# Performance work log

Hardware: AMD Instinct MI355X
Metric: run time of the kernel (lower is better)

## Reference

```python
import jax, jax.numpy as jnp
import numpy as np

NFEATS = 768; NHIDS = 768; H = 8; HD = NHIDS // H
NT = 32768; NC = 32768; NS = 32768; DEG = 8; E = NT * DEG
ALPHA = 0.2  # LeakyReLU negative slope


def setup_inputs() -> dict:
    key = jax.random.key(0)
    ks = jax.random.split(key, 16)
    f32 = jnp.float32
    dst = jnp.repeat(jnp.arange(NT, dtype=jnp.int32), DEG)  # uniform in-degree mailbox
    return {
        'h': jax.random.normal(ks[0], (NT, NFEATS), f32),
        'hb_c_src': jax.random.normal(ks[1], (NC, NHIDS), f32),
        'hb_s_src': jax.random.normal(ks[2], (NS, NHIDS), f32),
        'Wg': jax.random.normal(ks[3], (H, NFEATS, HD), f32) * 0.05,
        'bg': jnp.zeros((H, HD), f32),
        'ag': jax.random.normal(ks[4], (H, 2 * HD), f32) * 0.1,
        'agb': jnp.zeros((H,), f32),
        'Wx': jax.random.normal(ks[5], (H, NHIDS, HD), f32) * 0.05,
        'bx': jnp.zeros((H, HD), f32),
        'ax': jax.random.normal(ks[6], (H, 2 * HD), f32) * 0.1,
        'axb': jnp.zeros((H,), f32),
        'Wih': jax.random.normal(ks[7], (3 * NHIDS, NHIDS), f32) * 0.02,
        'Whh': jax.random.normal(ks[8], (3 * NHIDS, NHIDS), f32) * 0.02,
        'bih': jnp.zeros((3 * NHIDS,), f32),
        'bhh': jnp.zeros((3 * NHIDS,), f32),
        'intra_src': jax.random.randint(ks[9], (E,), 0, NT, jnp.int32),
        'intra_dst': dst,
        'c_src': jax.random.randint(ks[10], (E,), 0, NC, jnp.int32),
        'c_dst': dst,
        's_src': jax.random.randint(ks[11], (E,), 0, NS, jnp.int32),
        's_dst': dst,
    }


def _attend(Wh_s, Wh_d, src, dst, a, ab, n_dst):
    """Multi-head GAT edge attention + segment softmax + weighted aggregation.
    Wh_s: [Ns,H,D] src projections, Wh_d: [Nd,H,D] dst projections.
    a([Wh_src||Wh_dst]) decomposed as a_src.Wh_src + a_dst.Wh_dst + bias."""
    D = Wh_s.shape[-1]
    e = (jnp.einsum('nhd,hd->nh', Wh_s, a[:, :D])[src]
         + jnp.einsum('nhd,hd->nh', Wh_d, a[:, D:])[dst] + ab)  # [E,H]
    e = jax.nn.leaky_relu(e, ALPHA)
    m = jax.ops.segment_max(e, dst, num_segments=n_dst)
    ex = jnp.exp(e - m[dst])
    den = jax.ops.segment_sum(ex, dst, num_segments=n_dst)
    att = ex / den[dst]  # per-dst softmax over incoming edges (DGL mailbox softmax)
    out = jax.ops.segment_sum(Wh_s[src] * att[..., None], dst, num_segments=n_dst)
    return out.reshape(n_dst, H * D)  # concat heads


def _forward(h, hb_c_src, hb_s_src, Wg, bg, ag, agb, Wx, bx, ax, axb,
             Wih, Whh, bih, bhh, intra_src, intra_dst, c_src, c_dst, s_src, s_dst):
    n = h.shape[0]
    # intra-turn GAT (x = self.gat(g, t)); dropout is identity in eval mode
    Wh = jnp.einsum('nf,hfd->nhd', h, Wg) + bg
    x = _attend(Wh, Wh, intra_src, intra_dst, ag, agb, n)
    # cross-turn inversed GAT; dst nodes' 'hb' feature is the fresh gat output x;
    # counter_bw and support_bw share the same xgat weights.
    Wx_d = jnp.einsum('nf,hfd->nhd', x, Wx) + bx
    Wc_s = jnp.einsum('nf,hfd->nhd', hb_c_src, Wx) + bx
    h_c = _attend(Wc_s, Wx_d, c_src, c_dst, ax, axb, n)
    Ws_s = jnp.einsum('nf,hfd->nhd', hb_s_src, Wx) + bx
    h_s = _attend(Ws_s, Wx_d, s_src, s_dst, ax, axb, n)
    hid = 0.5 * h_c + 0.5 * h_s
    # GRUCell(x, hid)
    gi = x @ Wih.T + bih
    gh = hid @ Whh.T + bhh
    ir, iz, inn = jnp.split(gi, 3, axis=1)
    hr, hz, hn = jnp.split(gh, 3, axis=1)
    r = jax.nn.sigmoid(ir + hr)
    z = jax.nn.sigmoid(iz + hz)
    cand = jnp.tanh(inn + r * hn)
    return (1.0 - z) * cand + z * hid


def reference(h, hb_c_src, hb_s_src, Wg, bg, ag, agb, Wx, bx, ax, axb,
              Wih, Whh, bih, bhh, intra_src, intra_dst, c_src, c_dst, s_src, s_dst):
    return _forward(h, hb_c_src, hb_s_src, Wg, bg, ag, agb, Wx, bx, ax, axb,
                    Wih, Whh, bih, bhh, intra_src, intra_dst, c_src, c_dst, s_src, s_dst)
```

## Files before the change

kernel.cpp:

```cpp
#include <hip/hip_runtime.h>
#include <hip/hip_bf16.h>
#include <math.h>

#define NT 32768
#define HD 96
#define DEG 8
#define NE (NT * DEG)
#define LRELU_ALPHA 0.2f
#define CH 16384

typedef __attribute__((ext_vector_type(8))) short bf16x8;
typedef __attribute__((ext_vector_type(8))) unsigned short u16x8;
typedef __attribute__((ext_vector_type(4))) unsigned short u16x4;
typedef __attribute__((ext_vector_type(4))) float f32x4;

__device__ __forceinline__ unsigned short f2bf(float x) {
    union { float f; unsigned u; } v; v.f = x;
    unsigned r = v.u + 0x7FFFu + ((v.u >> 16) & 1u);
    return (unsigned short)(r >> 16);
}
__device__ __forceinline__ float bf2f(unsigned short u) {
    union { unsigned u; float f; } v; v.u = ((unsigned)u) << 16; return v.f;
}

__device__ __forceinline__ void gload_lds16(const void* g, void* l) {
    __builtin_amdgcn_global_load_lds(
        (const __attribute__((address_space(1))) void*)g,
        (__attribute__((address_space(3))) void*)l, 16, 0, 0);
}


__global__ void packWT(const float* __restrict__ W, unsigned short* __restrict__ T) {
    int idx = blockIdx.x * 256 + threadIdx.x;
    if (idx >= 768 * 768) return;
    int c = idx / 768, f = idx % 768;
    T[idx] = f2bf(W[(size_t)(c / HD) * 768 * HD + (size_t)f * HD + (c % HD)]);
}

__global__ void cvt_bf8(const float* __restrict__ X, unsigned short* __restrict__ Y, int n8) {
    int i = blockIdx.x * 256 + threadIdx.x;
    if (i >= n8) return;
    float4 a = ((const float4*)X)[2 * i];
    float4 b = ((const float4*)X)[2 * i + 1];
    u16x8 p;
    p[0] = f2bf(a.x); p[1] = f2bf(a.y); p[2] = f2bf(a.z); p[3] = f2bf(a.w);
    p[4] = f2bf(b.x); p[5] = f2bf(b.y); p[6] = f2bf(b.z); p[7] = f2bf(b.w);
    ((u16x8*)Y)[i] = p;
}

__global__ void packWV(const float* __restrict__ Wx, const float* __restrict__ ax,
                       const float* __restrict__ bx,
                       float* __restrict__ wv, float* __restrict__ cd) {
    int idx = blockIdx.x * 256 + threadIdx.x;
    if (idx < 8 * 768) {
        int h = idx / 768, f = idx % 768;
        const float* wp = Wx + (size_t)h * 768 * HD + (size_t)f * HD;
        const float* ap = ax + h * 2 * HD + HD;
        float s = 0.f;
        for (int d = 0; d < HD; d++) s += wp[d] * ap[d];
        wv[idx] = s;
    }
    if (idx < 8) {
        const float* bp = bx + idx * HD;
        const float* ap = ax + idx * 2 * HD + HD;
        float s = 0.f;
        for (int d = 0; d < HD; d++) s += bp[d] * ap[d];
        cd[idx] = s;
    }
}

__global__ __launch_bounds__(256, 4) void mgemm2(
    const unsigned short* __restrict__ A1, const unsigned short* __restrict__ A2,
    const unsigned short* __restrict__ BT1, const unsigned short* __restrict__ BT2,
    const float* __restrict__ bias1, const float* __restrict__ bias2,
    unsigned short* __restrict__ C1, unsigned short* __restrict__ C2,
    int mt1, int N, int K) {
    __shared__ unsigned short Alds[2][128 * 32];
    __shared__ unsigned short Blds[2][128 * 32];
    const int tid = threadIdx.x;
    const int w = tid >> 6, l = tid & 63;
    const int wr = w >> 1, wc = w & 1;
    const int lrow = l & 15, lk = l >> 4;

    const int nx = gridDim.x;
    const int nwg = nx * gridDim.y;
    int lin = blockIdx.y * nx + blockIdx.x;
    if ((nwg & 7) == 0) lin = (lin & 7) * (nwg >> 3) + (lin >> 3);
    int bm = lin / nx;
    const int bn = lin % nx;

    const bool p1 = bm < mt1;
    const unsigned short* A  = p1 ? A1 : A2;
    const unsigned short* BT = p1 ? BT1 : BT2;
    const float* bias        = p1 ? bias1 : bias2;
    unsigned short* C        = p1 ? C1 : C2;
    if (!p1) bm -= mt1;

    const unsigned short* asrc[2];
    const unsigned short* bsrc[2];
    #pragma unroll
    for (int q = 0; q < 2; q++) {
        int idx = q * 256 + tid;
        int r = idx >> 2, s = idx & 3;
        int kw = s ^ ((r >> 1) & 3);
        asrc[q] = A  + (size_t)(bm * 128 + r) * K + kw * 8;
        bsrc[q] = BT + (size_t)(bn * 128 + r) * K + kw * 8;
    }
    const int ldst = (w * 64) * 8;

    gload_lds16(asrc[0], &Alds[0][ldst]);
    gload_lds16(asrc[1], &Alds[0][2048 + ldst]);
    gload_lds16(bsrc[0], &Blds[0][ldst]);
    gload_lds16(bsrc[1], &Blds[0][2048 + ldst]);

    f32x4 acc[4][4] = {};
    const int nt = K >> 5;

    for (int t = 0; t < nt; ++t) {
        const int cur = t & 1;
        __syncthreads();
        if (t + 1 < nt) {
            const int k1 = (t + 1) << 5;
            gload_lds16(asrc[0] + k1, &Alds[cur ^ 1][ldst]);
            gload_lds16(asrc[1] + k1, &Alds[cur ^ 1][2048 + ldst]);
            gload_lds16(bsrc[0] + k1, &Blds[cur ^ 1][ldst]);
            gload_lds16(bsrc[1] + k1, &Blds[cur ^ 1][2048 + ldst]);
        }
        bf16x8 af[4], bfv[4];
        #pragma unroll
        for (int i = 0; i < 4; i++) {
            int r = wr * 64 + i * 16 + lrow;
            int s = lk ^ ((r >> 1) & 3);
            af[i] = *(const bf16x8*)(&Alds[cur][r * 32 + s * 8]);
        }
        #pragma unroll
        for (int j = 0; j < 4; j++) {
            int r = wc * 64 + j * 16 + lrow;
            int s = lk ^ ((r >> 1) & 3);
            bfv[j] = *(const bf16x8*)(&Blds[cur][r * 32 + s * 8]);
        }
        #pragma unroll
        for (int i = 0; i < 4; i++)
            #pragma unroll
            for (int j = 0; j < 4; j++)
                acc[i][j] = __builtin_amdgcn_mfma_f32_16x16x32_bf16(af[i], bfv[j], acc[i][j], 0, 0, 0);
    }

    const size_t crow0 = (size_t)bm * 128 + wr * 64;
    const int ccol0 = bn * 128 + wc * 64;
    #pragma unroll
    for (int j = 0; j < 4; j++) {
        int col = ccol0 + j * 16 + lrow;
        float bv = bias[col];
        #pragma unroll
        for (int i = 0; i < 4; i++) {
            size_t row = crow0 + i * 16 + lk * 4;
            #pragma unroll
            for (int e = 0; e < 4; e++)
                C[(row + e) * N + col] = f2bf(acc[i][j][e] + bv);
        }
    }
}

__global__ __launch_bounds__(256) void escore2(
    const unsigned short* __restrict__ X, const float* __restrict__ a,
    float* __restrict__ s0out, float* __restrict__ s1out) {
    __shared__ float av0[768], av1[768];
    for (int t = threadIdx.x; t < 768; t += 256) {
        int hh = t / HD, d = t % HD;
        av0[t] = a[hh * 2 * HD + d];
        av1[t] = a[hh * 2 * HD + HD + d];
    }
    __syncthreads();
    int idx = blockIdx.x * 256 + threadIdx.x;
    int row = idx >> 3, hh = idx & 7;
    const unsigned short* xp = X + (size_t)row * 768 + hh * HD;
    const float* a0 = av0 + hh * HD;
    const float* a1 = av1 + hh * HD;
    float s0 = 0.f, s1 = 0.f;
    #pragma unroll
    for (int q = 0; q < 12; q++) {
        u16x8 v = *(const u16x8*)(xp + q * 8);
        #pragma unroll
        for (int e = 0; e < 8; e++) {
            float x = bf2f(v[e]);
            s0 += x * a0[q * 8 + e];
            s1 += x * a1[q * 8 + e];
        }
    }
    s0out[idx] = s0;
    s1out[idx] = s1;
}

__global__ __launch_bounds__(256) void escore(
    const unsigned short* __restrict__ X, const float* __restrict__ a,
    int half, float* __restrict__ sc) {
    __shared__ float av[768];
    for (int t = threadIdx.x; t < 768; t += 256) {
        int hh = t / HD, d = t % HD;
        av[t] = a[hh * 2 * HD + half * HD + d];
    }
    __syncthreads();
    int idx = blockIdx.x * 256 + threadIdx.x;
    int row = idx >> 3, hh = idx & 7;
    const unsigned short* xp = X + (size_t)row * 768 + hh * HD;
    const float* ap = av + hh * HD;
    float s = 0.f;
    #pragma unroll
    for (int q = 0; q < 12; q++) {
        u16x8 v = *(const u16x8*)(xp + q * 8);
        #pragma unroll
        for (int e = 0; e < 8; e++) s += bf2f(v[e]) * ap[q * 8 + e];
    }
    sc[idx] = s;
}

__global__ __launch_bounds__(256) void escore_fold(
    const unsigned short* __restrict__ X, const float* __restrict__ wv,
    const float* __restrict__ cd, float* __restrict__ ed) {
    __shared__ float wvs[8][8][97];
    __shared__ float cds[8];
    for (int i = threadIdx.x; i < 8 * 8 * 96; i += 256) {
        int j = i / (8 * 96); int r = i % (8 * 96); int h = r / 96; int t = r % 96;
        wvs[j][h][t] = wv[h * 768 + j * 96 + t];
    }
    if (threadIdx.x < 8) cds[threadIdx.x] = cd[threadIdx.x];
    __syncthreads();
    int idx = blockIdx.x * 256 + threadIdx.x;
    int n = idx >> 3, j = idx & 7;
    const unsigned short* xp = X + (size_t)n * 768 + j * 96;
    float p[8] = {};
    #pragma unroll
    for (int q = 0; q < 12; q++) {
        u16x8 v = *(const u16x8*)(xp + q * 8);
        #pragma unroll
        for (int e = 0; e < 8; e++) {
            float x = bf2f(v[e]);
            #pragma unroll
            for (int h = 0; h < 8; h++) p[h] += x * wvs[j][h][q * 8 + e];
        }
    }
    #pragma unroll
    for (int o = 1; o < 8; o <<= 1)
        #pragma unroll
        for (int h = 0; h < 8; h++) p[h] += __shfl_xor(p[h], o, 64);
    ed[(size_t)n * 8 + j] = p[j] + cds[j];
}

__global__ __launch_bounds__(256) void attend_agg(
    const unsigned short* __restrict__ Whs, const float* __restrict__ es,
    const float* __restrict__ ed, const float* __restrict__ ab,
    const int* __restrict__ src, const int* __restrict__ dst,
    unsigned short* __restrict__ out) {
    const int wv = threadIdx.x >> 6, l = threadIdx.x & 63;
    const int seg = blockIdx.x * 4 + wv;
    const int hh = l >> 3, j = l & 7;
    int sj = src[seg * 8 + j];
    int dnode = dst[seg * 8];
    float e = es[(size_t)sj * 8 + hh] + ed[(size_t)dnode * 8 + hh] + ab[hh];
    e = e > 0.f ? e : LRELU_ALPHA * e;
    float m = e;
    #pragma unroll
    for (int o = 1; o < 8; o <<= 1) m = fmaxf(m, __shfl_xor(m, o, 64));
    float ex = expf(e - m);
    float s = ex;
    #pragma unroll
    for (int o = 1; o < 8; o <<= 1) s += __shfl_xor(s, o, 64);
    float att = ex / s;

    #pragma unroll
    for (int u = 0; u < 3; u++) {
        int c = 4 * l + 256 * u;
        int h = c / HD;
        float acc0 = 0.f, acc1 = 0.f, acc2 = 0.f, acc3 = 0.f;
        #pragma unroll
        for (int j2 = 0; j2 < 8; j2++) {
            float a = __shfl(att, h * 8 + j2, 64);
            int sid = __shfl(sj, j2, 64);
            u16x4 v = *(const u16x4*)(Whs + (size_t)sid * 768 + c);
            acc0 += a * bf2f(v[0]); acc1 += a * bf2f(v[1]);
            acc2 += a * bf2f(v[2]); acc3 += a * bf2f(v[3]);
        }
        u16x4 r;
        r[0] = f2bf(acc0); r[1] = f2bf(acc1); r[2] = f2bf(acc2); r[3] = f2bf(acc3);
        *(u16x4*)(out + (size_t)dnode * 768 + c) = r;
    }
}

__global__ __launch_bounds__(256) void attend2(
    const unsigned short* __restrict__ Wc, const unsigned short* __restrict__ Ws,
    const float* __restrict__ esC, const float* __restrict__ esS,
    const float* __restrict__ ed, const float* __restrict__ ab,
    const int* __restrict__ csrc, const int* __restrict__ ssrc,
    const int* __restrict__ dst, unsigned short* __restrict__ outH) {
    const int wv = threadIdx.x >> 6, l = threadIdx.x & 63;
    const int seg = blockIdx.x * 4 + wv;
    const int hh = l >> 3, j = l & 7;
    int cj = csrc[seg * 8 + j];
    int sj = ssrc[seg * 8 + j];
    int dnode = dst[seg * 8];
    float edv = ed[(size_t)dnode * 8 + hh] + ab[hh];

    float eC = esC[(size_t)cj * 8 + hh] + edv;
    eC = eC > 0.f ? eC : LRELU_ALPHA * eC;
    float mC = eC;
    #pragma unroll
    for (int o = 1; o < 8; o <<= 1) mC = fmaxf(mC, __shfl_xor(mC, o, 64));
    float exC = expf(eC - mC);
    float sC = exC;
    #pragma unroll
    for (int o = 1; o < 8; o <<= 1) sC += __shfl_xor(sC, o, 64);
    float attC = exC / sC;

    float eS = esS[(size_t)sj * 8 + hh] + edv;
    eS = eS > 0.f ? eS : LRELU_ALPHA * eS;
    float mS = eS;
    #pragma unroll
    for (int o = 1; o < 8; o <<= 1) mS = fmaxf(mS, __shfl_xor(mS, o, 64));
    float exS = expf(eS - mS);
    float sS = exS;
    #pragma unroll
    for (int o = 1; o < 8; o <<= 1) sS += __shfl_xor(sS, o, 64);
    float attS = exS / sS;

    #pragma unroll
    for (int u = 0; u < 3; u++) {
        int c = 4 * l + 256 * u;
        int h = c / HD;
        float acc0 = 0.f, acc1 = 0.f, acc2 = 0.f, acc3 = 0.f;
        #pragma unroll
        for (int j2 = 0; j2 < 8; j2++) {
            float a = __shfl(attC, h * 8 + j2, 64);
            int sid = __shfl(cj, j2, 64);
            u16x4 v = *(const u16x4*)(Wc + (size_t)sid * 768 + c);
            acc0 += a * bf2f(v[0]); acc1 += a * bf2f(v[1]);
            acc2 += a * bf2f(v[2]); acc3 += a * bf2f(v[3]);
        }
        #pragma unroll
        for (int j2 = 0; j2 < 8; j2++) {
            float a = __shfl(attS, h * 8 + j2, 64);
            int sid = __shfl(sj, j2, 64);
            u16x4 v = *(const u16x4*)(Ws + (size_t)sid * 768 + c);
            acc0 += a * bf2f(v[0]); acc1 += a * bf2f(v[1]);
            acc2 += a * bf2f(v[2]); acc3 += a * bf2f(v[3]);
        }
        u16x4 r;
        r[0] = f2bf(0.5f * acc0); r[1] = f2bf(0.5f * acc1);
        r[2] = f2bf(0.5f * acc2); r[3] = f2bf(0.5f * acc3);
        *(u16x4*)(outH + (size_t)dnode * 768 + c) = r;
    }
}

__global__ __launch_bounds__(256) void gru_elem(
    const unsigned short* __restrict__ gi, const unsigned short* __restrict__ gh,
    const unsigned short* __restrict__ hid, float* __restrict__ out) {
    int idx = blockIdx.x * 256 + threadIdx.x;
    int nrow = idx / 96, c8 = (idx % 96) * 8;
    const unsigned short* gip = gi + (size_t)nrow * 2304 + c8;
    const unsigned short* ghp = gh + (size_t)nrow * 2304 + c8;
    u16x8 vir = *(const u16x8*)(gip);
    u16x8 viz = *(const u16x8*)(gip + 768);
    u16x8 vin = *(const u16x8*)(gip + 1536);
    u16x8 vhr = *(const u16x8*)(ghp);
    u16x8 vhz = *(const u16x8*)(ghp + 768);
    u16x8 vhn = *(const u16x8*)(ghp + 1536);
    u16x8 vh  = *(const u16x8*)(hid + (size_t)nrow * 768 + c8);
    float res[8];
    #pragma unroll
    for (int e = 0; e < 8; e++) {
        float r = 1.f / (1.f + expf(-(bf2f(vir[e]) + bf2f(vhr[e]))));
        float z = 1.f / (1.f + expf(-(bf2f(viz[e]) + bf2f(vhz[e]))));
        float cand = tanhf(bf2f(vin[e]) + r * bf2f(vhn[e]));
        res[e] = (1.f - z) * cand + z * bf2f(vh[e]);
    }
    float* op = out + (size_t)nrow * 768 + c8;
    *(float4*)(op)     = make_float4(res[0], res[1], res[2], res[3]);
    *(float4*)(op + 4) = make_float4(res[4], res[5], res[6], res[7]);
}

extern "C" void kernel_launch(void* const* d_in, const int* in_sizes, int n_in,
                              void* d_out, int out_size, void* d_ws, size_t ws_size,
                              hipStream_t stream) {
    const float* h    = (const float*)d_in[0];
    const float* hbc  = (const float*)d_in[1];
    const float* hbs  = (const float*)d_in[2];
    const float* Wg   = (const float*)d_in[3];
    const float* bg   = (const float*)d_in[4];
    const float* ag   = (const float*)d_in[5];
    const float* agb  = (const float*)d_in[6];
    const float* Wx   = (const float*)d_in[7];
    const float* bx   = (const float*)d_in[8];
    const float* ax   = (const float*)d_in[9];
    const float* axb  = (const float*)d_in[10];
    const float* Wih  = (const float*)d_in[11];
    const float* Whh  = (const float*)d_in[12];
    const float* bih  = (const float*)d_in[13];
    const float* bhh  = (const float*)d_in[14];
    const int* i_src  = (const int*)d_in[15];
    const int* i_dst  = (const int*)d_in[16];
    const int* c_src  = (const int*)d_in[17];
    const int* c_dst  = (const int*)d_in[18];
    const int* s_src  = (const int*)d_in[19];
    const int* s_dst  = (const int*)d_in[20];
    float* out = (float*)d_out;

    const size_t SZ = (size_t)NT * 768;
    unsigned short* Xb   = (unsigned short*)d_ws;
    unsigned short* Hdb  = Xb + SZ;
    unsigned short* GIb  = Hdb + SZ;
    unsigned short* GHb  = GIb + (size_t)CH * 2304;
    unsigned short* ABh  = GIb;
    unsigned short* ABc  = GIb + SZ;
    unsigned short* ABs  = GIb + 2 * SZ;
    unsigned short* W2gT = GHb + (size_t)CH * 2304;
    unsigned short* W2xT = W2gT + 768 * 768;
    unsigned short* WihB = W2xT + 768 * 768;
    unsigned short* WhhB = WihB + 2304 * 768;
    float* EScat = (float*)(WhhB + 2304 * 768);
    float* ED    = EScat + 2 * NE;
    float* ESI   = ED + NE;
    float* EDI   = ESI + NE;
    float* WV    = EDI + NE;
    float* CD    = WV + 8 * 768;
    unsigned short* Pcat = (unsigned short*)d_out;

    dim3 blk(256);
    packWT<<<(768 * 768 + 255) / 256, blk, 0, stream>>>(Wg, W2gT);
    packWT<<<(768 * 768 + 255) / 256, blk, 0, stream>>>(Wx, W2xT);
    cvt_bf8<<<(2304 * 768 / 8 + 255) / 256, blk, 0, stream>>>(Wih, WihB, 2304 * 768 / 8);
    cvt_bf8<<<(2304 * 768 / 8 + 255) / 256, blk, 0, stream>>>(Whh, WhhB, 2304 * 768 / 8);
    packWV<<<(8 * 768 + 255) / 256, blk, 0, stream>>>(Wx, ax, bx, WV, CD);

    const int n8 = (int)(SZ / 8);
    const int cvtg = (n8 + 255) / 256;

    cvt_bf8<<<cvtg, blk, 0, stream>>>(h,   ABh, n8);
    cvt_bf8<<<cvtg, blk, 0, stream>>>(hbc, ABc, n8);
    cvt_bf8<<<cvtg, blk, 0, stream>>>(hbs, ABs, n8);

    dim3 gproj(6, 768);
    mgemm2<<<gproj, blk, 0, stream>>>(ABh, ABc, W2gT, W2xT, bg, bx,
                                      Hdb, Pcat, 256, 768, 768);
    escore2<<<NE / 256, blk, 0, stream>>>(Hdb, ag, ESI, EDI);
    attend_agg<<<NT / 4, blk, 0, stream>>>(Hdb, ESI, EDI, agb, i_src, i_dst, Xb);
    escore_fold<<<NE / 256, blk, 0, stream>>>(Xb, WV, CD, ED);
    escore<<<2 * NE / 256, blk, 0, stream>>>(Pcat, ax, 0, EScat);
    attend2<<<NT / 4, blk, 0, stream>>>(Pcat, Pcat + SZ, EScat, EScat + NE, ED, axb,
                                        c_src, s_src, c_dst, Hdb);
    dim3 ggru(18, 256);
    for (int c0 = 0; c0 < NT; c0 += CH) {
        mgemm2<<<ggru, blk, 0, stream>>>(Xb + (size_t)c0 * 768, Hdb + (size_t)c0 * 768,
                                         WihB, WhhB, bih, bhh, GIb, GHb,
                                         128, 2304, 768);
        gru_elem<<<(CH * 96) / 256, blk, 0, stream>>>(GIb, GHb, Hdb + (size_t)c0 * 768, out + (size_t)c0 * 768);
    }
}
```

Measured before the change: 913.4 us.

## Fuse fp32-to-bf16 input conversion into projection GEMM; load A fragments directly

Removes the three separate cvt_bf8 passes over h, hb_c_src and hb_s_src. The projection GEMM now reads fp32 rows straight from global memory and converts them to bf16 in registers, covering all three inputs in one launch. The GRU GEMM also skips LDS staging for the A operand and loads MFMA fragments directly from global memory. This saves the conversion passes, their bf16 intermediates and the LDS traffic for A. In exchange, A loads are no longer coalesced, are not double-buffered, and 16 B columns may be re-read redundantly across waves.

```diff
diff --git a/kernel.cpp b/kernel.cpp
--- a/kernel.cpp
+++ b/kernel.cpp
@@ -69,13 +69,14 @@
     }
 }
 
-__global__ __launch_bounds__(256, 4) void mgemm2(
-    const unsigned short* __restrict__ A1, const unsigned short* __restrict__ A2,
+__global__ __launch_bounds__(256, 4) void mgemm3f(
+    const float* __restrict__ A1, const float* __restrict__ A2,
+    const float* __restrict__ A3,
     const unsigned short* __restrict__ BT1, const unsigned short* __restrict__ BT2,
     const float* __restrict__ bias1, const float* __restrict__ bias2,
     unsigned short* __restrict__ C1, unsigned short* __restrict__ C2,
-    int mt1, int N, int K) {
-    __shared__ unsigned short Alds[2][128 * 32];
+    unsigned short* __restrict__ C3,
+    int mt1, int mt2, int N, int K) {
     __shared__ unsigned short Blds[2][128 * 32];
     const int tid = threadIdx.x;
     const int w = tid >> 6, l = tid & 63;
@@ -89,6 +90,100 @@
     int bm = lin / nx;
     const int bn = lin % nx;
 
+    const int part = (bm >= mt1) + (bm >= mt2);
+    const float* A            = part == 0 ? A1 : (part == 1 ? A2 : A3);
+    const unsigned short* BT  = part == 0 ? BT1 : BT2;
+    const float* bias         = part == 0 ? bias1 : bias2;
+    unsigned short* C         = part == 0 ? C1 : (part == 1 ? C2 : C3);
+    bm -= (part == 1 ? mt1 : (part == 2 ? mt2 : 0));
+
+    const unsigned short* bsrc[2];
+    #pragma unroll
+    for (int q = 0; q < 2; q++) {
+        int idx = q * 256 + tid;
+        int r = idx >> 2, s = idx & 3;
+        int kw = s ^ ((r >> 1) & 3);
+        bsrc[q] = BT + (size_t)(bn * 128 + r) * K + kw * 8;
+    }
+    const int ldst = (w * 64) * 8;
+
+    const float* aRow[4];
+    #pragma unroll
+    for (int i = 0; i < 4; i++)
+        aRow[i] = A + (size_t)(bm * 128 + wr * 64 + i * 16 + lrow) * K + lk * 8;
+
+    gload_lds16(bsrc[0], &Blds[0][ldst]);
+    gload_lds16(bsrc[1], &Blds[0][2048 + ldst]);
+
+    f32x4 acc[4][4] = {};
+    const int nt = K >> 5;
+
+    for (int t = 0; t < nt; ++t) {
+        const int cur = t & 1;
+        __syncthreads();
+        if (t + 1 < nt) {
+            const int k1 = (t + 1) << 5;
+            gload_lds16(bsrc[0] + k1, &Blds[cur ^ 1][ldst]);
+            gload_lds16(bsrc[1] + k1, &Blds[cur ^ 1][2048 + ldst]);
+        }
+        bf16x8 af[4], bfv[4];
+        #pragma unroll
+        for (int i = 0; i < 4; i++) {
+            float4 x = *(const float4*)(aRow[i] + t * 32);
+            float4 y = *(const float4*)(aRow[i] + t * 32 + 4);
+            u16x8 p;
+            p[0] = f2bf(x.x); p[1] = f2bf(x.y); p[2] = f2bf(x.z); p[3] = f2bf(x.w);
+            p[4] = f2bf(y.x); p[5] = f2bf(y.y); p[6] = f2bf(y.z); p[7] = f2bf(y.w);
+            af[i] = (bf16x8)p;
+        }
+        #pragma unroll
+        for (int j = 0; j < 4; j++) {
+            int r = wc * 64 + j * 16 + lrow;
+            int s = lk ^ ((r >> 1) & 3);
+            bfv[j] = *(const bf16x8*)(&Blds[cur][r * 32 + s * 8]);
+        }
+        #pragma unroll
+        for (int i = 0; i < 4; i++)
+            #pragma unroll
+            for (int j = 0; j < 4; j++)
+                acc[i][j] = __builtin_amdgcn_mfma_f32_16x16x32_bf16(af[i], bfv[j], acc[i][j], 0, 0, 0);
+    }
+
+    const size_t crow0 = (size_t)bm * 128 + wr * 64;
+    const int ccol0 = bn * 128 + wc * 64;
+    #pragma unroll
+    for (int j = 0; j < 4; j++) {
+        int col = ccol0 + j * 16 + lrow;
+        float bv = bias[col];
+        #pragma unroll
+        for (int i = 0; i < 4; i++) {
+            size_t row = crow0 + i * 16 + lk * 4;
+            #pragma unroll
+            for (int e = 0; e < 4; e++)
+                C[(row + e) * N + col] = f2bf(acc[i][j][e] + bv);
+        }
+    }
+}
+
+__global__ __launch_bounds__(256, 4) void mgemm2b(
+    const unsigned short* __restrict__ A1, const unsigned short* __restrict__ A2,
+    const unsigned short* __restrict__ BT1, const unsigned short* __restrict__ BT2,
+    const float* __restrict__ bias1, const float* __restrict__ bias2,
+    unsigned short* __restrict__ C1, unsigned short* __restrict__ C2,
+    int mt1, int N, int K) {
+    __shared__ unsigned short Blds[2][128 * 32];
+    const int tid = threadIdx.x;
+    const int w = tid >> 6, l = tid & 63;
+    const int wr = w >> 1, wc = w & 1;
+    const int lrow = l & 15, lk = l >> 4;
+
+    const int nx = gridDim.x;
+    const int nwg = nx * gridDim.y;
+    int lin = blockIdx.y * nx + blockIdx.x;
+    if ((nwg & 7) == 0) lin = (lin & 7) * (nwg >> 3) + (lin >> 3);
+    int bm = lin / nx;
+    const int bn = lin % nx;
+
     const bool p1 = bm < mt1;
     const unsigned short* A  = p1 ? A1 : A2;
     const unsigned short* BT = p1 ? BT1 : BT2;
@@ -96,20 +191,21 @@
     unsigned short* C        = p1 ? C1 : C2;
     if (!p1) bm -= mt1;
 
-    const unsigned short* asrc[2];
     const unsigned short* bsrc[2];
     #pragma unroll
     for (int q = 0; q < 2; q++) {
         int idx = q * 256 + tid;
         int r = idx >> 2, s = idx & 3;
         int kw = s ^ ((r >> 1) & 3);
-        asrc[q] = A  + (size_t)(bm * 128 + r) * K + kw * 8;
         bsrc[q] = BT + (size_t)(bn * 128 + r) * K + kw * 8;
     }
     const int ldst = (w * 64) * 8;
 
-    gload_lds16(asrc[0], &Alds[0][ldst]);
-    gload_lds16(asrc[1], &Alds[0][2048 + ldst]);
+    const unsigned short* aRow[4];
+    #pragma unroll
+    for (int i = 0; i < 4; i++)
+        aRow[i] = A + (size_t)(bm * 128 + wr * 64 + i * 16 + lrow) * K + lk * 8;
+
     gload_lds16(bsrc[0], &Blds[0][ldst]);
     gload_lds16(bsrc[1], &Blds[0][2048 + ldst]);
 
@@ -121,18 +217,13 @@
         __syncthreads();
         if (t + 1 < nt) {
             const int k1 = (t + 1) << 5;
-            gload_lds16(asrc[0] + k1, &Alds[cur ^ 1][ldst]);
-            gload_lds16(asrc[1] + k1, &Alds[cur ^ 1][2048 + ldst]);
             gload_lds16(bsrc[0] + k1, &Blds[cur ^ 1][ldst]);
             gload_lds16(bsrc[1] + k1, &Blds[cur ^ 1][2048 + ldst]);
         }
         bf16x8 af[4], bfv[4];
         #pragma unroll
-        for (int i = 0; i < 4; i++) {
-            int r = wr * 64 + i * 16 + lrow;
-            int s = lk ^ ((r >> 1) & 3);
-            af[i] = *(const bf16x8*)(&Alds[cur][r * 32 + s * 8]);
-        }
+        for (int i = 0; i < 4; i++)
+            af[i] = *(const bf16x8*)(aRow[i] + t * 32);
         #pragma unroll
         for (int j = 0; j < 4; j++) {
             int r = wc * 64 + j * 16 + lrow;
@@ -409,9 +500,6 @@
     unsigned short* Hdb  = Xb + SZ;
     unsigned short* GIb  = Hdb + SZ;
     unsigned short* GHb  = GIb + (size_t)CH * 2304;
-    unsigned short* ABh  = GIb;
-    unsigned short* ABc  = GIb + SZ;
-    unsigned short* ABs  = GIb + 2 * SZ;
     unsigned short* W2gT = GHb + (size_t)CH * 2304;
     unsigned short* W2xT = W2gT + 768 * 768;
     unsigned short* WihB = W2xT + 768 * 768;
@@ -431,16 +519,9 @@
     cvt_bf8<<<(2304 * 768 / 8 + 255) / 256, blk, 0, stream>>>(Whh, WhhB, 2304 * 768 / 8);
     packWV<<<(8 * 768 + 255) / 256, blk, 0, stream>>>(Wx, ax, bx, WV, CD);
 
-    const int n8 = (int)(SZ / 8);
-    const int cvtg = (n8 + 255) / 256;
-
-    cvt_bf8<<<cvtg, blk, 0, stream>>>(h,   ABh, n8);
-    cvt_bf8<<<cvtg, blk, 0, stream>>>(hbc, ABc, n8);
-    cvt_bf8<<<cvtg, blk, 0, stream>>>(hbs, ABs, n8);
-
     dim3 gproj(6, 768);
-    mgemm2<<<gproj, blk, 0, stream>>>(ABh, ABc, W2gT, W2xT, bg, bx,
-                                      Hdb, Pcat, 256, 768, 768);
+    mgemm3f<<<gproj, blk, 0, stream>>>(h, hbc, hbs, W2gT, W2xT, bg, bx,
+                                       Hdb, Pcat, Pcat + SZ, 256, 512, 768, 768);
     escore2<<<NE / 256, blk, 0, stream>>>(Hdb, ag, ESI, EDI);
     attend_agg<<<NT / 4, blk, 0, stream>>>(Hdb, ESI, EDI, agb, i_src, i_dst, Xb);
     escore_fold<<<NE / 256, blk, 0, stream>>>(Xb, WV, CD, ED);
@@ -449,9 +530,9 @@
                                         c_src, s_src, c_dst, Hdb);
     dim3 ggru(18, 256);
     for (int c0 = 0; c0 < NT; c0 += CH) {
-        mgemm2<<<ggru, blk, 0, stream>>>(Xb + (size_t)c0 * 768, Hdb + (size_t)c0 * 768,
-                                         WihB, WhhB, bih, bhh, GIb, GHb,
-                                         128, 2304, 768);
+        mgemm2b<<<ggru, blk, 0, stream>>>(Xb + (size_t)c0 * 768, Hdb + (size_t)c0 * 768,
+                                          WihB, WhhB, bih, bhh, GIb, GHb,
+                                          128, 2304, 768);
         gru_elem<<<(CH * 96) / 256, blk, 0, stream>>>(GIb, GHb, Hdb + (size_t)c0 * 768, out + (size_t)c0 * 768);
     }
 }
```

New measurement: 1.341 ms. 1.47x slower.

## Fuse folded dst-score into attend_agg epilogue and merge escore kernels

Applied to the files above, without the earlier changes.

The folded destination-score computation for cross attention (x·(Wx·a_dst)) moves into the intra-GAT aggregation kernel. It uses the fp32 accumulators and a transposed WV layout, followed by a wave-wide shuffle reduction, so Xb no longer has to be re-read in a separate pass. The three escore launches merge into one kernel that dispatches on block index. This cuts one full-tensor read and a few launches, at the cost of extra FMAs and a 6-step by 8-value shuffle reduction per wave in attend_agg. It also computes scores from unrounded fp32 values instead of the bf16-rounded ones.

```diff
diff --git a/kernel.cpp b/kernel.cpp
--- a/kernel.cpp
+++ b/kernel.cpp
@@ -48,9 +48,9 @@
     ((u16x8*)Y)[i] = p;
 }
 
-__global__ void packWV(const float* __restrict__ Wx, const float* __restrict__ ax,
-                       const float* __restrict__ bx,
-                       float* __restrict__ wv, float* __restrict__ cd) {
+__global__ void packWVT(const float* __restrict__ Wx, const float* __restrict__ ax,
+                        const float* __restrict__ bx,
+                        float* __restrict__ wvT, float* __restrict__ cd) {
     int idx = blockIdx.x * 256 + threadIdx.x;
     if (idx < 8 * 768) {
         int h = idx / 768, f = idx % 768;
@@ -58,7 +58,7 @@
         const float* ap = ax + h * 2 * HD + HD;
         float s = 0.f;
         for (int d = 0; d < HD; d++) s += wp[d] * ap[d];
-        wv[idx] = s;
+        wvT[(size_t)f * 8 + h] = s;
     }
     if (idx < 8) {
         const float* bp = bx + idx * HD;
@@ -162,96 +162,62 @@
     }
 }
 
-__global__ __launch_bounds__(256) void escore2(
-    const unsigned short* __restrict__ X, const float* __restrict__ a,
-    float* __restrict__ s0out, float* __restrict__ s1out) {
-    __shared__ float av0[768], av1[768];
+__global__ __launch_bounds__(256) void escore_all(
+    const unsigned short* __restrict__ Xd, const unsigned short* __restrict__ Xs,
+    const float* __restrict__ ag, const float* __restrict__ ax,
+    float* __restrict__ s0out, float* __restrict__ s1out,
+    float* __restrict__ sout) {
+    __shared__ float av0[768], av1[768], axs[768];
     for (int t = threadIdx.x; t < 768; t += 256) {
         int hh = t / HD, d = t % HD;
-        av0[t] = a[hh * 2 * HD + d];
-        av1[t] = a[hh * 2 * HD + HD + d];
+        av0[t] = ag[hh * 2 * HD + d];
+        av1[t] = ag[hh * 2 * HD + HD + d];
+        axs[t] = ax[hh * 2 * HD + d];
     }
     __syncthreads();
-    int idx = blockIdx.x * 256 + threadIdx.x;
-    int row = idx >> 3, hh = idx & 7;
-    const unsigned short* xp = X + (size_t)row * 768 + hh * HD;
-    const float* a0 = av0 + hh * HD;
-    const float* a1 = av1 + hh * HD;
-    float s0 = 0.f, s1 = 0.f;
-    #pragma unroll
-    for (int q = 0; q < 12; q++) {
-        u16x8 v = *(const u16x8*)(xp + q * 8);
-        #pragma unroll
-        for (int e = 0; e < 8; e++) {
-            float x = bf2f(v[e]);
-            s0 += x * a0[q * 8 + e];
-            s1 += x * a1[q * 8 + e];
-        }
-    }
-    s0out[idx] = s0;
-    s1out[idx] = s1;
-}
-
-__global__ __launch_bounds__(256) void escore(
-    const unsigned short* __restrict__ X, const float* __restrict__ a,
-    int half, float* __restrict__ sc) {
-    __shared__ float av[768];
-    for (int t = threadIdx.x; t < 768; t += 256) {
-        int hh = t / HD, d = t % HD;
-        av[t] = a[hh * 2 * HD + half * HD + d];
-    }
-    __syncthreads();
-    int idx = blockIdx.x * 256 + threadIdx.x;
-    int row = idx >> 3, hh = idx & 7;
-    const unsigned short* xp = X + (size_t)row * 768 + hh * HD;
-    const float* ap = av + hh * HD;
-    float s = 0.f;
-    #pragma unroll
-    for (int q = 0; q < 12; q++) {
-        u16x8 v = *(const u16x8*)(xp + q * 8);
-        #pragma unroll
-        for (int e = 0; e < 8; e++) s += bf2f(v[e]) * ap[q * 8 + e];
-    }
-    sc[idx] = s;
-}
-
-__global__ __launch_bounds__(256) void escore_fold(
-    const unsigned short* __restrict__ X, const float* __restrict__ wv,
-    const float* __restrict__ cd, float* __restrict__ ed) {
-    __shared__ float wvs[8][8][97];
-    __shared__ float cds[8];
-    for (int i = threadIdx.x; i < 8 * 8 * 96; i += 256) {
-        int j = i / (8 * 96); int r = i % (8 * 96); int h = r / 96; int t = r % 96;
-        wvs[j][h][t] = wv[h * 768 + j * 96 + t];
-    }
-    if (threadIdx.x < 8) cds[threadIdx.x] = cd[threadIdx.x];
-    __syncthreads();
-    int idx = blockIdx.x * 256 + threadIdx.x;
-    int n = idx >> 3, j = idx & 7;
-    const unsigned short* xp = X + (size_t)n * 768 + j * 96;
-    float p[8] = {};
-    #pragma unroll
-    for (int q = 0; q < 12; q++) {
-        u16x8 v = *(const u16x8*)(xp + q * 8);
-        #pragma unroll
-        for (int e = 0; e < 8; e++) {
-            float x = bf2f(v[e]);
+    const int NB0 = NE / 256;
+    if ((int)blockIdx.x < NB0) {
+        int idx = blockIdx.x * 256 + threadIdx.x;
+        int row = idx >> 3, hh = idx & 7;
+        const unsigned short* xp = Xd + (size_t)row * 768 + hh * HD;
+        const float* a0 = av0 + hh * HD;
+        const float* a1 = av1 + hh * HD;
+        float s0 = 0.f, s1 = 0.f;
+        #pragma unroll
+        for (int q = 0; q < 12; q++) {
+            u16x8 v = *(const u16x8*)(xp + q * 8);
             #pragma unroll
-            for (int h = 0; h < 8; h++) p[h] += x * wvs[j][h][q * 8 + e];
-        }
-    }
-    #pragma unroll
-    for (int o = 1; o < 8; o <<= 1)
-        #pragma unroll
-        for (int h = 0; h < 8; h++) p[h] += __shfl_xor(p[h], o, 64);
-    ed[(size_t)n * 8 + j] = p[j] + cds[j];
+            for (int e = 0; e < 8; e++) {
+                float x = bf2f(v[e]);
+                s0 += x * a0[q * 8 + e];
+                s1 += x * a1[q * 8 + e];
+            }
+        }
+        s0out[idx] = s0;
+        s1out[idx] = s1;
+    } else {
+        int idx = (blockIdx.x - NB0) * 256 + threadIdx.x;
+        int row = idx >> 3, hh = idx & 7;
+        const unsigned short* xp = Xs + (size_t)row * 768 + hh * HD;
+        const float* ap = axs + hh * HD;
+        float s = 0.f;
+        #pragma unroll
+        for (int q = 0; q < 12; q++) {
+            u16x8 v = *(const u16x8*)(xp + q * 8);
+            #pragma unroll
+            for (int e = 0; e < 8; e++) s += bf2f(v[e]) * ap[q * 8 + e];
+        }
+        sout[idx] = s;
+    }
 }
 
 __global__ __launch_bounds__(256) void attend_agg(
     const unsigned short* __restrict__ Whs, const float* __restrict__ es,
     const float* __restrict__ ed, const float* __restrict__ ab,
     const int* __restrict__ src, const int* __restrict__ dst,
-    unsigned short* __restrict__ out) {
+    unsigned short* __restrict__ out,
+    const float* __restrict__ wvT, const float* __restrict__ cd,
+    float* __restrict__ edout) {
     const int wv = threadIdx.x >> 6, l = threadIdx.x & 63;
     const int seg = blockIdx.x * 4 + wv;
     const int hh = l >> 3, j = l & 7;
@@ -268,6 +234,7 @@
     for (int o = 1; o < 8; o <<= 1) s += __shfl_xor(s, o, 64);
     float att = ex / s;
 
+    float p8[8] = {};
     #pragma unroll
     for (int u = 0; u < 3; u++) {
         int c = 4 * l + 256 * u;
@@ -284,6 +251,29 @@
         u16x4 r;
         r[0] = f2bf(acc0); r[1] = f2bf(acc1); r[2] = f2bf(acc2); r[3] = f2bf(acc3);
         *(u16x4*)(out + (size_t)dnode * 768 + c) = r;
+        float xs[4] = {acc0, acc1, acc2, acc3};
+        #pragma unroll
+        for (int jj = 0; jj < 4; jj++) {
+            const float* wp = wvT + (size_t)(c + jj) * 8;
+            float4 w0 = *(const float4*)wp;
+            float4 w1 = *(const float4*)(wp + 4);
+            p8[0] += xs[jj] * w0.x; p8[1] += xs[jj] * w0.y;
+            p8[2] += xs[jj] * w0.z; p8[3] += xs[jj] * w0.w;
+            p8[4] += xs[jj] * w1.x; p8[5] += xs[jj] * w1.y;
+            p8[6] += xs[jj] * w1.z; p8[7] += xs[jj] * w1.w;
+        }
+    }
+    #pragma unroll
+    for (int o = 1; o < 64; o <<= 1) {
+        #pragma unroll
+        for (int k = 0; k < 8; k++) p8[k] += __shfl_xor(p8[k], o, 64);
+    }
+    if (l == 0) {
+        float4 c0 = *(const float4*)cd;
+        float4 c1 = *(const float4*)(cd + 4);
+        float* op = edout + (size_t)dnode * 8;
+        *(float4*)op       = make_float4(p8[0] + c0.x, p8[1] + c0.y, p8[2] + c0.z, p8[3] + c0.w);
+        *(float4*)(op + 4) = make_float4(p8[4] + c1.x, p8[5] + c1.y, p8[6] + c1.z, p8[7] + c1.w);
     }
 }
 
@@ -420,8 +410,8 @@
     float* ED    = EScat + 2 * NE;
     float* ESI   = ED + NE;
     float* EDI   = ESI + NE;
-    float* WV    = EDI + NE;
-    float* CD    = WV + 8 * 768;
+    float* WVT   = EDI + NE;
+    float* CD    = WVT + 768 * 8;
     unsigned short* Pcat = (unsigned short*)d_out;
 
     dim3 blk(256);
@@ -429,7 +419,7 @@
     packWT<<<(768 * 768 + 255) / 256, blk, 0, stream>>>(Wx, W2xT);
     cvt_bf8<<<(2304 * 768 / 8 + 255) / 256, blk, 0, stream>>>(Wih, WihB, 2304 * 768 / 8);
     cvt_bf8<<<(2304 * 768 / 8 + 255) / 256, blk, 0, stream>>>(Whh, WhhB, 2304 * 768 / 8);
-    packWV<<<(8 * 768 + 255) / 256, blk, 0, stream>>>(Wx, ax, bx, WV, CD);
+    packWVT<<<(8 * 768 + 255) / 256, blk, 0, stream>>>(Wx, ax, bx, WVT, CD);
 
     const int n8 = (int)(SZ / 8);
     const int cvtg = (n8 + 255) / 256;
@@ -441,10 +431,10 @@
     dim3 gproj(6, 768);
     mgemm2<<<gproj, blk, 0, stream>>>(ABh, ABc, W2gT, W2xT, bg, bx,
                                       Hdb, Pcat, 256, 768, 768);
-    escore2<<<NE / 256, blk, 0, stream>>>(Hdb, ag, ESI, EDI);
-    attend_agg<<<NT / 4, blk, 0, stream>>>(Hdb, ESI, EDI, agb, i_src, i_dst, Xb);
-    escore_fold<<<NE / 256, blk, 0, stream>>>(Xb, WV, CD, ED);
-    escore<<<2 * NE / 256, blk, 0, stream>>>(Pcat, ax, 0, EScat);
+    escore_all<<<3 * NE / 256, blk, 0, stream>>>(Hdb, Pcat, ag, ax,
+                                                 ESI, EDI, EScat);
+    attend_agg<<<NT / 4, blk, 0, stream>>>(Hdb, ESI, EDI, agb, i_src, i_dst, Xb,
+                                           WVT, CD, ED);
     attend2<<<NT / 4, blk, 0, stream>>>(Pcat, Pcat + SZ, EScat, EScat + NE, ED, axb,
                                         c_src, s_src, c_dst, Hdb);
     dim3 ggru(18, 256);
```

Result: no change. 929.1 us (+1.7%).
